# Optimization experiments

Measured on AMD Instinct MI355X. Metric: run time of the kernel, lower is better.

## Reference

```python
import jax, jax.numpy as jnp
import numpy as np

B, N, K = 4096, 10000, 100

def setup_inputs() -> dict:
    key = jax.random.key(0)
    k1, k2 = jax.random.split(key)
    nodes = jax.random.uniform(k1, (B, N, 2), dtype=jnp.float32)
    candidate_indices = jax.random.randint(k2, (B, K), 0, N, dtype=jnp.int64)
    return {"nodes": nodes, "candidate_indices": candidate_indices}

def reference(nodes, candidate_indices):
    # nodes: [B, N, 2], candidate_indices: [B, K] with -1 = padding
    valid = candidate_indices != -1                      # [B, K]
    safe_idx = jnp.where(valid, candidate_indices, 0)    # [B, K]
    # gather candidate coords: [B, K, 2]
    cand = jnp.take_along_axis(
        nodes, jnp.broadcast_to(safe_idx[:, :, None], safe_idx.shape + (2,)), axis=1)
    big = jnp.asarray(jnp.inf, nodes.dtype)
    x = cand[:, :, 0]
    y = cand[:, :, 1]
    x_min = jnp.min(jnp.where(valid, x,  big), axis=1)   # [B]
    x_max = jnp.max(jnp.where(valid, x, -big), axis=1)
    y_min = jnp.min(jnp.where(valid, y,  big), axis=1)
    y_max = jnp.max(jnp.where(valid, y, -big), axis=1)
    span = jnp.maximum(x_max - x_min, y_max - y_min)
    r = 1.0 / jnp.clip(span, 1e-6)                       # [B]
    mins = jnp.stack([x_min, y_min], axis=-1)            # [B, 2]
    normalized = jnp.clip(r[:, None, None] * (nodes - mins[:, None, :]), 0.0, 1.0)
    any_valid = jnp.any(valid, axis=1)                   # [B]
    return jnp.where(any_valid[:, None, None], normalized, nodes)
```

## Files before the change

kernel.cpp:

```cpp
#include <hip/hip_runtime.h>
#include <math.h>

#define BATCH 4096
#define NNODES 10000
#define KCAND 100
#define F4_PER_BATCH (NNODES * 2 / 4)

typedef float f4 __attribute__((ext_vector_type(4)));

__global__ __launch_bounds__(256) void fused_normalize_kernel(
        const float* __restrict__ nodes,
        const int* __restrict__ cand,
        float* __restrict__ out) {
    const int b = blockIdx.x;
    const int tid = threadIdx.x;
    const int wave = tid >> 6;
    const int lane = tid & 63;

    const float* nb = nodes + (size_t)b * (NNODES * 2);

    float xmin =  INFINITY, xmax = -INFINITY;
    float ymin =  INFINITY, ymax = -INFINITY;
    float any = 0.0f;

    if (tid < KCAND) {
        int id = cand[(size_t)b * KCAND + tid];
        if (id != -1) {
            any = 1.0f;
            const float2 p = *reinterpret_cast<const float2*>(nb + (size_t)id * 2);
            xmin = p.x; xmax = p.x;
            ymin = p.y; ymax = p.y;
        }
    }

    #pragma unroll
    for (int off = 32; off > 0; off >>= 1) {
        xmin = fminf(xmin, __shfl_xor(xmin, off, 64));
        xmax = fmaxf(xmax, __shfl_xor(xmax, off, 64));
        ymin = fminf(ymin, __shfl_xor(ymin, off, 64));
        ymax = fmaxf(ymax, __shfl_xor(ymax, off, 64));
        any  = fmaxf(any,  __shfl_xor(any,  off, 64));
    }

    __shared__ float sxmin[4], sxmax[4], symin[4], symax[4], sany[4];
    if (lane == 0) {
        sxmin[wave] = xmin; sxmax[wave] = xmax;
        symin[wave] = ymin; symax[wave] = ymax;
        sany[wave]  = any;
    }
    __syncthreads();

    xmin = fminf(fminf(sxmin[0], sxmin[1]), fminf(sxmin[2], sxmin[3]));
    xmax = fmaxf(fmaxf(sxmax[0], sxmax[1]), fmaxf(sxmax[2], sxmax[3]));
    ymin = fminf(fminf(symin[0], symin[1]), fminf(symin[2], symin[3]));
    ymax = fmaxf(fmaxf(symax[0], symax[1]), fmaxf(symax[2], symax[3]));
    any  = fmaxf(fmaxf(sany[0],  sany[1]),  fmaxf(sany[2],  sany[3]));

    const float span = fmaxf(xmax - xmin, ymax - ymin);
    const float r = 1.0f / fmaxf(span, 1e-6f);
    const bool valid = (any != 0.0f);

    const f4* src = reinterpret_cast<const f4*>(nb);
    f4* dst = reinterpret_cast<f4*>(out + (size_t)b * (NNODES * 2));

    if (valid) {
        for (int i = tid; i < F4_PER_BATCH; i += 256) {
            f4 v = __builtin_nontemporal_load(src + i);
            v.x = fminf(fmaxf(r * (v.x - xmin), 0.0f), 1.0f);
            v.y = fminf(fmaxf(r * (v.y - ymin), 0.0f), 1.0f);
            v.z = fminf(fmaxf(r * (v.z - xmin), 0.0f), 1.0f);
            v.w = fminf(fmaxf(r * (v.w - ymin), 0.0f), 1.0f);
            __builtin_nontemporal_store(v, dst + i);
        }
    } else {
        for (int i = tid; i < F4_PER_BATCH; i += 256) {
            f4 v = __builtin_nontemporal_load(src + i);
            __builtin_nontemporal_store(v, dst + i);
        }
    }
}

extern "C" void kernel_launch(void* const* d_in, const int* in_sizes, int n_in,
                              void* d_out, int out_size, void* d_ws, size_t ws_size,
                              hipStream_t stream) {
    const float* nodes = (const float*)d_in[0];
    const int* cand = (const int*)d_in[1];
    float* out = (float*)d_out;

    fused_normalize_kernel<<<dim3(BATCH), dim3(256), 0, stream>>>(nodes, cand, out);
}
```

Before: 127.2 us.

## Prefetch streaming tiles before the candidate reduction and software-pipeline the loop

Each thread now issues the first four vector loads of its node slice before the min/max reduction and barrier, so the main streaming traffic overlaps the candidate gather latency. The main loop is fully unrolled over 20 iterations with a rotating four-entry register buffer that keeps loads in flight ahead of use. The candidate gather is made branchless, and the normalization becomes an fma with a precomputed bias. The cost is higher register pressure, and fma rounding can differ slightly from subtract-then-multiply.

```diff
diff --git a/kernel.cpp b/kernel.cpp
--- a/kernel.cpp
+++ b/kernel.cpp
@@ -4,7 +4,9 @@
 #define BATCH 4096
 #define NNODES 10000
 #define KCAND 100
-#define F4_PER_BATCH (NNODES * 2 / 4)
+#define F4_PER_BATCH 5000
+#define NITER 20
+#define PF 4
 
 typedef float f4 __attribute__((ext_vector_type(4)));
 
@@ -18,20 +20,26 @@
     const int lane = tid & 63;
 
     const float* nb = nodes + (size_t)b * (NNODES * 2);
+    const f4* src = reinterpret_cast<const f4*>(nb);
+    f4* dst = reinterpret_cast<f4*>(out + (size_t)b * (NNODES * 2));
 
-    float xmin =  INFINITY, xmax = -INFINITY;
-    float ymin =  INFINITY, ymax = -INFINITY;
-    float any = 0.0f;
+    const int cidx = tid < KCAND ? tid : (KCAND - 1);
+    const int id = cand[(size_t)b * KCAND + cidx];
+    const bool valid = (tid < KCAND) && (id != -1);
+    const int safe = valid ? id : 0;
+    const float2 p = *reinterpret_cast<const float2*>(nb + (size_t)safe * 2);
 
-    if (tid < KCAND) {
-        int id = cand[(size_t)b * KCAND + tid];
-        if (id != -1) {
-            any = 1.0f;
-            const float2 p = *reinterpret_cast<const float2*>(nb + (size_t)id * 2);
-            xmin = p.x; xmax = p.x;
-            ymin = p.y; ymax = p.y;
-        }
+    f4 buf[PF];
+    #pragma unroll
+    for (int j = 0; j < PF; ++j) {
+        buf[j] = __builtin_nontemporal_load(src + tid + j * 256);
     }
+
+    float xmin = valid ? p.x :  INFINITY;
+    float xmax = valid ? p.x : -INFINITY;
+    float ymin = valid ? p.y :  INFINITY;
+    float ymax = valid ? p.y : -INFINITY;
+    float any  = valid ? 1.0f : 0.0f;
 
     #pragma unroll
     for (int off = 32; off > 0; off >>= 1) {
@@ -42,40 +50,40 @@
         any  = fmaxf(any,  __shfl_xor(any,  off, 64));
     }
 
-    __shared__ float sxmin[4], sxmax[4], symin[4], symax[4], sany[4];
+    __shared__ float sred[5][4];
     if (lane == 0) {
-        sxmin[wave] = xmin; sxmax[wave] = xmax;
-        symin[wave] = ymin; symax[wave] = ymax;
-        sany[wave]  = any;
+        sred[0][wave] = xmin; sred[1][wave] = xmax;
+        sred[2][wave] = ymin; sred[3][wave] = ymax;
+        sred[4][wave] = any;
     }
     __syncthreads();
-
-    xmin = fminf(fminf(sxmin[0], sxmin[1]), fminf(sxmin[2], sxmin[3]));
-    xmax = fmaxf(fmaxf(sxmax[0], sxmax[1]), fmaxf(sxmax[2], sxmax[3]));
-    ymin = fminf(fminf(symin[0], symin[1]), fminf(symin[2], symin[3]));
-    ymax = fmaxf(fmaxf(symax[0], symax[1]), fmaxf(symax[2], symax[3]));
-    any  = fmaxf(fmaxf(sany[0],  sany[1]),  fmaxf(sany[2],  sany[3]));
+    xmin = fminf(fminf(sred[0][0], sred[0][1]), fminf(sred[0][2], sred[0][3]));
+    xmax = fmaxf(fmaxf(sred[1][0], sred[1][1]), fmaxf(sred[1][2], sred[1][3]));
+    ymin = fminf(fminf(sred[2][0], sred[2][1]), fminf(sred[2][2], sred[2][3]));
+    ymax = fmaxf(fmaxf(sred[3][0], sred[3][1]), fmaxf(sred[3][2], sred[3][3]));
+    any  = fmaxf(fmaxf(sred[4][0], sred[4][1]), fmaxf(sred[4][2], sred[4][3]));
 
     const float span = fmaxf(xmax - xmin, ymax - ymin);
     const float r = 1.0f / fmaxf(span, 1e-6f);
-    const bool valid = (any != 0.0f);
+    const bool ok = (any != 0.0f);
+    const float bx = -r * xmin;
+    const float by = -r * ymin;
 
-    const f4* src = reinterpret_cast<const f4*>(nb);
-    f4* dst = reinterpret_cast<f4*>(out + (size_t)b * (NNODES * 2));
-
-    if (valid) {
-        for (int i = tid; i < F4_PER_BATCH; i += 256) {
-            f4 v = __builtin_nontemporal_load(src + i);
-            v.x = fminf(fmaxf(r * (v.x - xmin), 0.0f), 1.0f);
-            v.y = fminf(fmaxf(r * (v.y - ymin), 0.0f), 1.0f);
-            v.z = fminf(fmaxf(r * (v.z - xmin), 0.0f), 1.0f);
-            v.w = fminf(fmaxf(r * (v.w - ymin), 0.0f), 1.0f);
-            __builtin_nontemporal_store(v, dst + i);
-        }
-    } else {
-        for (int i = tid; i < F4_PER_BATCH; i += 256) {
-            f4 v = __builtin_nontemporal_load(src + i);
-            __builtin_nontemporal_store(v, dst + i);
+    #pragma unroll
+    for (int it = 0; it < NITER; ++it) {
+        const int i = tid + it * 256;
+        const int ipf = i + PF * 256;
+        f4 v = buf[it & (PF - 1)];
+        if (ipf < F4_PER_BATCH)
+            buf[it & (PF - 1)] = __builtin_nontemporal_load(src + ipf);
+        if (i < F4_PER_BATCH) {
+            f4 o;
+            o.x = fminf(fmaxf(fmaf(r, v.x, bx), 0.0f), 1.0f);
+            o.y = fminf(fmaxf(fmaf(r, v.y, by), 0.0f), 1.0f);
+            o.z = fminf(fmaxf(fmaf(r, v.z, bx), 0.0f), 1.0f);
+            o.w = fminf(fmaxf(fmaf(r, v.w, by), 0.0f), 1.0f);
+            if (!ok) o = v;
+            __builtin_nontemporal_store(o, dst + i);
         }
     }
 }
```

Result: faster. 118.2 us (-7.1%).
